# Performance work log

Measured on AMD Instinct MI355X. Metric: run time of the kernel, lower is better.

The kernel has to match this reference:

```python
import jax, jax.numpy as jnp
import numpy as np

B, T, E, H, HS, L, V = 128, 256, 384, 6, 64, 6, 78
FF = 4 * E  # 1536


def layer_norm(x, g, b, eps=1e-5):
    mu = jnp.mean(x, axis=-1, keepdims=True)
    var = jnp.mean((x - mu) ** 2, axis=-1, keepdims=True)
    return (x - mu) * jax.lax.rsqrt(var + eps) * g + b


def setup_inputs() -> dict:
    key = jax.random.key(0)
    ks = jax.random.split(key, 20)
    s = 0.02
    return {
        "context": jax.random.randint(ks[0], (B, T), 0, V),
        "tok_emb": jax.random.normal(ks[1], (V, E)) * s,
        "pos_emb": jax.random.normal(ks[2], (T, E)) * s,
        "ln1_g": jnp.ones((L, E)), "ln1_b": jnp.zeros((L, E)),
        "w_qkv": jax.random.normal(ks[3], (L, H, E, 3 * HS)) * s,  # per-head qkv, no bias
        "w_proj": jax.random.normal(ks[4], (L, E, E)) * s,
        "b_proj": jnp.zeros((L, E)),
        "ln2_g": jnp.ones((L, E)), "ln2_b": jnp.zeros((L, E)),
        "w1": jax.random.normal(ks[5], (L, E, FF)) * s, "b1": jnp.zeros((L, FF)),
        "w2": jax.random.normal(ks[6], (L, FF, E)) * s, "b2": jnp.zeros((L, E)),
        "lnf_g": jnp.ones((E,)), "lnf_b": jnp.zeros((E,)),
        "w_head": jax.random.normal(ks[7], (E, V)) * s, "b_head": jnp.zeros((V,)),
    }


def reference(context, tok_emb, pos_emb, ln1_g, ln1_b, w_qkv, w_proj, b_proj,
              ln2_g, ln2_b, w1, b1, w2, b2, lnf_g, lnf_b, w_head, b_head):
    x = tok_emb[context] + pos_emb[None, :, :]            # [B,T,E]
    causal = jnp.tril(jnp.ones((T, T), dtype=bool))       # lower-tri mask
    scale = HS ** (-0.5)
    for l in range(L):
        # multi-head attention (pre-LN), per-head qkv projection, no bias
        xn = layer_norm(x, ln1_g[l], ln1_b[l])
        qkv = jnp.einsum('bte,hef->bthf', xn, w_qkv[l])   # [B,T,H,3*HS]
        q, k, v = jnp.split(qkv, 3, axis=-1)              # each [B,T,H,HS]
        scores = jnp.einsum('bthd,bshd->bhts', q, k) * scale
        scores = jnp.where(causal, scores, -jnp.inf)
        att = jax.nn.softmax(scores, axis=-1)             # [B,H,T,T]
        o = jnp.einsum('bhts,bshd->bthd', att, v).reshape(B, T, E)
        x = x + o @ w_proj[l] + b_proj[l]
        # feed-forward (pre-LN)
        xn2 = layer_norm(x, ln2_g[l], ln2_b[l])
        x = x + jax.nn.relu(xn2 @ w1[l] + b1[l]) @ w2[l] + b2[l]
    x = layer_norm(x, lnf_g, lnf_b)
    return x @ w_head + b_head                            # [B,T,V]
```

## Files before the change

kernel.cpp:

```cpp
#include <hip/hip_runtime.h>


#define Bc 128
#define Tc 256
#define Ec 384
#define Hc 6
#define HSc 64
#define Lc 6
#define Vc 78
#define FFc 1536
#define Mc (Bc * Tc)

typedef unsigned short u16;
using bf16x8 = __attribute__((ext_vector_type(8))) short;
using f32x4 = __attribute__((ext_vector_type(4))) float;

__device__ __forceinline__ float b2f(u16 u) {
    union { float f; unsigned int i; } x;
    x.i = ((unsigned int)u) << 16;
    return x.f;
}
__device__ __forceinline__ u16 f2b(float f) {
    union { float f; unsigned int u; } x;
    x.f = f;
    unsigned int r = x.u + 0x7fffu + ((x.u >> 16) & 1u);
    return (u16)(r >> 16);
}

__device__ __forceinline__ void gload_lds16(const u16* g, u16* l) {
    __builtin_amdgcn_global_load_lds(
        (const __attribute__((address_space(1))) unsigned int*)g,
        (__attribute__((address_space(3))) unsigned int*)l, 16, 0, 0);
}

__global__ __launch_bounds__(256) void poison_kernel(
    float* __restrict__ out, int n, float val) {
    int i = blockIdx.x * 256 + threadIdx.x;
    if (i < n) out[i] = val;
}

__global__ __launch_bounds__(256) void trans_qkv_kernel(
    const float* __restrict__ in, u16* __restrict__ out) {
    int i = blockIdx.x * 256 + threadIdx.x;
    if (i >= Lc * Hc * Ec * 192) return;
    int f = i % 192;
    int r = i / 192;
    int e = r % Ec; r /= Ec;
    int h = r % Hc;
    int l = r / Hc;
    out[((size_t)l * 1152 + h * 192 + f) * Ec + e] = f2b(in[i]);
}
__global__ __launch_bounds__(256) void trans_w_kernel(
    const float* __restrict__ in, u16* __restrict__ out, int K, int N) {
    int i = blockIdx.x * 256 + threadIdx.x;
    if (i >= Lc * K * N) return;
    int n = i % N;
    int r = i / N;
    int k = r % K;
    int l = r / K;
    out[((size_t)l * N + n) * K + k] = f2b(in[i]);
}
__global__ __launch_bounds__(256) void trans_head_kernel(
    const float* __restrict__ in, u16* __restrict__ out) {
    int i = blockIdx.x * 256 + threadIdx.x;
    if (i >= Ec * Vc) return;
    int v = i % Vc, e = i / Vc;
    out[(size_t)v * Ec + e] = f2b(in[i]);
}

__global__ __launch_bounds__(256) void embed_kernel(
    const int* __restrict__ ctx, const float* __restrict__ tok,
    const float* __restrict__ pos, float* __restrict__ x) {
    int i = blockIdx.x * 256 + threadIdx.x;
    if (i >= Mc * 96) return;
    int c4 = (i % 96) * 4, bt = i / 96, t = bt % Tc;
    f32x4 tv = *reinterpret_cast<const f32x4*>(&tok[ctx[bt] * Ec + c4]);
    f32x4 pv = *reinterpret_cast<const f32x4*>(&pos[t * Ec + c4]);
    *reinterpret_cast<f32x4*>(&x[(size_t)bt * Ec + c4]) = tv + pv;
}

__global__ __launch_bounds__(256) void ln_kernel(
    const float* __restrict__ X, u16* __restrict__ Y,
    const float* __restrict__ g, const float* __restrict__ b, int nrows) {
    int row = blockIdx.x * 4 + (threadIdx.x >> 6);
    int lane = threadIdx.x & 63;
    if (row >= nrows) return;
    const float* xr = X + (size_t)row * Ec;
    float2 v[3];
    float s = 0.f;
#pragma unroll
    for (int i = 0; i < 3; ++i) {
        v[i] = *reinterpret_cast<const float2*>(&xr[2 * lane + 128 * i]);
        s += v[i].x + v[i].y;
    }
#pragma unroll
    for (int off = 32; off >= 1; off >>= 1) s += __shfl_xor(s, off, 64);
    float mean = s * (1.0f / Ec);
    float s2 = 0.f;
#pragma unroll
    for (int i = 0; i < 3; ++i) {
        float dx = v[i].x - mean, dy = v[i].y - mean;
        s2 += dx * dx + dy * dy;
    }
#pragma unroll
    for (int off = 32; off >= 1; off >>= 1) s2 += __shfl_xor(s2, off, 64);
    float rstd = rsqrtf(s2 * (1.0f / Ec) + 1e-5f);
    u16* yr = Y + (size_t)row * Ec;
#pragma unroll
    for (int i = 0; i < 3; ++i) {
        int e = 2 * lane + 128 * i;
        float2 gv = *reinterpret_cast<const float2*>(&g[e]);
        float2 bv = *reinterpret_cast<const float2*>(&b[e]);
        ushort2 ov;
        ov.x = f2b((v[i].x - mean) * rstd * gv.x + bv.x);
        ov.y = f2b((v[i].y - mean) * rstd * gv.y + bv.y);
        *reinterpret_cast<ushort2*>(&yr[e]) = ov;
    }
}

template <bool RELU, bool RESID, bool OUTBF16, bool VECEPI, bool PIPE3>
__global__ __launch_bounds__(256) void mfma_gemm(
    const u16* __restrict__ A, const u16* __restrict__ Wt,
    const float* __restrict__ bias, const float* R, void* C,
    int K, int ldC, int NV) {
    constexpr bool SWAP = VECEPI;
    __shared__ __align__(16) u16 smem[PIPE3 ? 24576 : 16384];
    int tid = threadIdx.x;

    int nwg = gridDim.x * gridDim.y;
    int bid = blockIdx.y * gridDim.x + blockIdx.x;
    int q = nwg >> 3, r = nwg & 7;
    int xcd = bid & 7, idx = bid >> 3;
    int swz = (xcd < r ? xcd * (q + 1) : r * (q + 1) + (xcd - r) * q) + idx;
    int bx = swz % gridDim.x, by = swz / gridDim.x;
    int m0 = by * 128, n0 = bx * 128;

    int w = tid >> 6, lane = tid & 63;
    int wm = (w >> 1) * 64, wn = (w & 1) * 64;
    int r16 = lane & 15, quad = lane >> 4;

    f32x4 acc[4][4] = {};

    if constexpr (PIPE3) {
        u16(*As3)[128][32] = (u16(*)[128][32])smem;
        u16(*Bs3)[128][32] = (u16(*)[128][32])(smem + 3 * 128 * 32);
        int rA = 2 * w * 16 + (lane >> 2);
        int colsw = ((lane & 3) ^ ((lane >> 3) & 3)) * 8;
        const u16* a0 = A + (size_t)(m0 + rA) * K + colsw;
        const u16* a1 = A + (size_t)(m0 + rA + 16) * K + colsw;
        const u16* b0 = Wt + (size_t)(n0 + rA) * K + colsw;
        const u16* b1 = Wt + (size_t)(n0 + rA + 16) * K + colsw;

        auto stage3 = [&](int buf, int t) {
            int k0 = t * 32;
            gload_lds16(a0 + k0, &As3[buf][2 * w * 16][0]);
            gload_lds16(a1 + k0, &As3[buf][2 * w * 16 + 16][0]);
            gload_lds16(b0 + k0, &Bs3[buf][2 * w * 16][0]);
            gload_lds16(b1 + k0, &Bs3[buf][2 * w * 16 + 16][0]);
        };
        int csw = (quad ^ ((r16 >> 1) & 3)) * 8;
        auto compute3 = [&](int buf) {
            bf16x8 af[4], bf[4];
#pragma unroll
            for (int i = 0; i < 4; ++i) {
                af[i] = *reinterpret_cast<const bf16x8*>(
                    &As3[buf][wm + i * 16 + r16][csw]);
                bf[i] = *reinterpret_cast<const bf16x8*>(
                    &Bs3[buf][wn + i * 16 + r16][csw]);
            }
#pragma unroll
            for (int mi = 0; mi < 4; ++mi)
#pragma unroll
                for (int ni = 0; ni < 4; ++ni) {
                    if (SWAP)
                        acc[mi][ni] = __builtin_amdgcn_mfma_f32_16x16x32_bf16(
                            bf[ni], af[mi], acc[mi][ni], 0, 0, 0);
                    else
                        acc[mi][ni] = __builtin_amdgcn_mfma_f32_16x16x32_bf16(
                            af[mi], bf[ni], acc[mi][ni], 0, 0, 0);
                }
        };

        int nt = K >> 5;
        stage3(0, 0);
        stage3(1, 1);
        int buf = 0;
        for (int t = 0; t < nt - 1; ++t) {
            asm volatile("s_waitcnt vmcnt(4)" ::: "memory");
            __builtin_amdgcn_s_barrier();
            __builtin_amdgcn_sched_barrier(0);
            if (t + 2 < nt) {
                int b2 = buf + 2;
                if (b2 >= 3) b2 -= 3;
                stage3(b2, t + 2);
            }
            compute3(buf);
            buf = (buf == 2) ? 0 : buf + 1;
        }
        asm volatile("s_waitcnt vmcnt(0)" ::: "memory");
        __builtin_amdgcn_s_barrier();
        __builtin_amdgcn_sched_barrier(0);
        compute3(buf);
    } else {
        u16(*As)[64] = (u16(*)[64])smem;
        u16(*Bs)[64] = (u16(*)[64])(smem + 128 * 64);
        int lrow = lane >> 3;
        int scol = ((lane & 7) ^ lrow) * 8;
        const u16* ap[4];
        const u16* bp[4];
#pragma unroll
        for (int j = 0; j < 4; ++j) {
            int row = (w * 4 + j) * 8 + lrow;
            ap[j] = A + (size_t)(m0 + row) * K + scol;
            bp[j] = Wt + (size_t)(n0 + row) * K + scol;
        }
        for (int k0 = 0; k0 < K; k0 += 64) {
            __syncthreads();
#pragma unroll
            for (int j = 0; j < 4; ++j) {
                gload_lds16(ap[j], &As[(w * 4 + j) * 8][0]);
                gload_lds16(bp[j], &Bs[(w * 4 + j) * 8][0]);
                ap[j] += 64;
                bp[j] += 64;
            }
            __syncthreads();
#pragma unroll
            for (int kk = 0; kk < 2; ++kk) {
                int csw = ((kk * 4 + quad) ^ (r16 & 7)) * 8;
                bf16x8 af[4], bf[4];
#pragma unroll
                for (int i = 0; i < 4; ++i) {
                    af[i] = *reinterpret_cast<const bf16x8*>(
                        &As[wm + i * 16 + r16][csw]);
                    bf[i] = *reinterpret_cast<const bf16x8*>(
                        &Bs[wn + i * 16 + r16][csw]);
                }
#pragma unroll
                for (int mi = 0; mi < 4; ++mi)
#pragma unroll
                    for (int ni = 0; ni < 4; ++ni) {
                        if (SWAP)
                            acc[mi][ni] = __builtin_amdgcn_mfma_f32_16x16x32_bf16(
                                bf[ni], af[mi], acc[mi][ni], 0, 0, 0);
                        else
                            acc[mi][ni] = __builtin_amdgcn_mfma_f32_16x16x32_bf16(
                                af[mi], bf[ni], acc[mi][ni], 0, 0, 0);
                    }
            }
        }
    }

    if (VECEPI && OUTBF16) {
        f32x4 bv4[4];
#pragma unroll
        for (int ni = 0; ni < 4; ++ni) {
            int gn = n0 + wn + ni * 16 + quad * 4;
            if (bias)
                bv4[ni] = *reinterpret_cast<const f32x4*>(&bias[gn]);
            else
                bv4[ni] = f32x4{0.f, 0.f, 0.f, 0.f};
        }
        __syncthreads();
#pragma unroll
        for (int mi = 0; mi < 4; ++mi) {
            int row = wm + mi * 16 + r16;
#pragma unroll
            for (int ni = 0; ni < 4; ++ni) {
                int colb = wn + ni * 16 + quad * 4;
                f32x4 v = acc[mi][ni] + bv4[ni];
                if (RELU) {
#pragma unroll
                    for (int e = 0; e < 4; ++e) v[e] = fmaxf(v[e], 0.f);
                }
                ushort4 ov;
                ov.x = f2b(v[0]);
                ov.y = f2b(v[1]);
                ov.z = f2b(v[2]);
                ov.w = f2b(v[3]);
                int pc = (colb >> 3) ^ (row & 15);
                *reinterpret_cast<ushort4*>(
                    &smem[row * 128 + pc * 8 + (colb & 7)]) = ov;
            }
        }
        __syncthreads();
        u16* cp = (u16*)C;
#pragma unroll
        for (int i = 0; i < 4; ++i) {
            int row = (tid >> 3) + 32 * i;
#pragma unroll
            for (int h = 0; h < 2; ++h) {
                int lc = (tid & 7) + 8 * h;
                int pc = lc ^ (row & 15);
                bf16x8 val = *reinterpret_cast<const bf16x8*>(
                    &smem[row * 128 + pc * 8]);
                *reinterpret_cast<bf16x8*>(
                    &cp[(size_t)(m0 + row) * ldC + n0 + lc * 8]) = val;
            }
        }
    } else if (VECEPI) {
        float* cp = (float*)C;
        f32x4 bv4[4];
#pragma unroll
        for (int ni = 0; ni < 4; ++ni) {
            int gn = n0 + wn + ni * 16 + quad * 4;
            if (bias)
                bv4[ni] = *reinterpret_cast<const f32x4*>(&bias[gn]);
            else
                bv4[ni] = f32x4{0.f, 0.f, 0.f, 0.f};
        }
#pragma unroll
        for (int mi = 0; mi < 4; ++mi) {
            int gm = m0 + wm + mi * 16 + r16;
#pragma unroll
            for (int ni = 0; ni < 4; ++ni) {
                int gn = n0 + wn + ni * 16 + quad * 4;
                size_t goff = (size_t)gm * ldC + gn;
                f32x4 v = acc[mi][ni] + bv4[ni];
                if (RELU) {
#pragma unroll
                    for (int e = 0; e < 4; ++e) v[e] = fmaxf(v[e], 0.f);
                }
                if (RESID) v += *reinterpret_cast<const f32x4*>(&R[goff]);
                *reinterpret_cast<f32x4*>(&cp[goff]) = v;
            }
        }
    } else {
#pragma unroll
        for (int mi = 0; mi < 4; ++mi)
#pragma unroll
            for (int ni = 0; ni < 4; ++ni) {
                int gn = n0 + wn + ni * 16 + r16;
                if (gn >= NV) continue;
                float bvs = bias ? bias[gn] : 0.f;
#pragma unroll
                for (int reg = 0; reg < 4; ++reg) {
                    int gm = m0 + wm + mi * 16 + quad * 4 + reg;
                    float v = acc[mi][ni][reg] + bvs;
                    if (RESID) v += R[(size_t)gm * ldC + gn];
                    if (RELU) v = fmaxf(v, 0.f);
                    if (OUTBF16)
                        ((u16*)C)[(size_t)gm * ldC + gn] = f2b(v);
                    else
                        ((float*)C)[(size_t)gm * ldC + gn] = v;
                }
            }
    }
}

__global__ __launch_bounds__(256) void attn_kernel(
    const u16* __restrict__ qkv, u16* __restrict__ o) {
    __shared__ u16 Qs[64][72];
    __shared__ u16 Ks[64][72];
    __shared__ u16 Vt[64][72];
    __shared__ u16 Ps[4][16][72];
    int tid = threadIdx.x;
    int tt = blockIdx.x, h = blockIdx.y, b = blockIdx.z;
    int w = tid >> 6, lane = tid & 63;
    int r16 = lane & 15, quad = lane >> 4;
    int t0 = tt * 64;
    const u16* base = qkv + (size_t)b * Tc * 1152 + h * 192;

    int sr = tid >> 2, sd = (tid & 3) * 16;
    {
        const u16* src = base + (size_t)(t0 + sr) * 1152 + sd;
        *reinterpret_cast<uint4*>(&Qs[sr][sd]) =
            *reinterpret_cast<const uint4*>(src);
        *reinterpret_cast<uint4*>(&Qs[sr][sd + 8]) =
            *reinterpret_cast<const uint4*>(src + 8);
    }
    __syncthreads();
    bf16x8 aq0 = *reinterpret_cast<const bf16x8*>(&Qs[w * 16 + r16][quad * 8]);
    bf16x8 aq1 = *reinterpret_cast<const bf16x8*>(&Qs[w * 16 + r16][32 + quad * 8]);

    uint4 kr0, kr1, vr0, vr1;
    {
        const u16* ks = base + (size_t)sr * 1152 + 64 + sd;
        kr0 = *reinterpret_cast<const uint4*>(ks);
        kr1 = *reinterpret_cast<const uint4*>(ks + 8);
        const u16* vs = base + (size_t)sr * 1152 + 128 + sd;
        vr0 = *reinterpret_cast<const uint4*>(vs);
        vr1 = *reinterpret_cast<const uint4*>(vs + 8);
    }
    int vslot = sr & 7, vchk = sr >> 3;

    float m_run[4], l_run[4];
#pragma unroll
    for (int r = 0; r < 4; ++r) { m_run[r] = -3.0e38f; l_run[r] = 0.f; }
    f32x4 acc_o[4] = {};

    for (int st = 0; st <= tt; ++st) {
        __syncthreads();
        {
            *reinterpret_cast<uint4*>(&Ks[sr][sd]) = kr0;
            *reinterpret_cast<uint4*>(&Ks[sr][sd + 8]) = kr1;
            u16 tv[16];
            *reinterpret_cast<uint4*>(tv) = vr0;
            *reinterpret_cast<uint4*>(tv + 8) = vr1;
#pragma unroll
            for (int j = 0; j < 16; ++j) {
                int row = sd + j;
                int pc = vchk ^ ((row >> 3) & 7);
                Vt[row][pc * 8 + vslot] = tv[j];
            }
        }
        __syncthreads();
        if (st < tt) {
            const u16* ks = base + (size_t)((st + 1) * 64 + sr) * 1152 + 64 + sd;
            kr0 = *reinterpret_cast<const uint4*>(ks);
            kr1 = *reinterpret_cast<const uint4*>(ks + 8);
            const u16* vs = base + (size_t)((st + 1) * 64 + sr) * 1152 + 128 + sd;
            vr0 = *reinterpret_cast<const uint4*>(vs);
            vr1 = *reinterpret_cast<const uint4*>(vs + 8);
        }

        f32x4 acc_s[4] = {};
#pragma unroll
        for (int ni = 0; ni < 4; ++ni) {
            bf16x8 bk0 = *reinterpret_cast<const bf16x8*>(&Ks[ni * 16 + r16][quad * 8]);
            bf16x8 bk1 = *reinterpret_cast<const bf16x8*>(&Ks[ni * 16 + r16][32 + quad * 8]);
            acc_s[ni] = __builtin_amdgcn_mfma_f32_16x16x32_bf16(aq0, bk0, acc_s[ni], 0, 0, 0);
            acc_s[ni] = __builtin_amdgcn_mfma_f32_16x16x32_bf16(aq1, bk1, acc_s[ni], 0, 0, 0);
        }

        float sc[4][4];
        float mt[4] = {-3.0e38f, -3.0e38f, -3.0e38f, -3.0e38f};
#pragma unroll
        for (int ni = 0; ni < 4; ++ni)
#pragma unroll
            for (int reg = 0; reg < 4; ++reg) {
                int col = st * 64 + ni * 16 + r16;
                int row = t0 + w * 16 + quad * 4 + reg;
                float v = (col <= row) ? acc_s[ni][reg] * 0.125f : -3.0e38f;
                sc[ni][reg] = v;
                mt[reg] = fmaxf(mt[reg], v);
            }
#pragma unroll
        for (int reg = 0; reg < 4; ++reg) {
#pragma unroll
            for (int off = 1; off <= 8; off <<= 1)
                mt[reg] = fmaxf(mt[reg], __shfl_xor(mt[reg], off, 64));
        }
        float alpha[4], lt[4];
#pragma unroll
        for (int reg = 0; reg < 4; ++reg) {
            float m_new = fmaxf(m_run[reg], mt[reg]);
            alpha[reg] = __expf(m_run[reg] - m_new);
            m_run[reg] = m_new;
            lt[reg] = 0.f;
        }
#pragma unroll
        for (int ni = 0; ni < 4; ++ni)
#pragma unroll
            for (int reg = 0; reg < 4; ++reg) {
                float p = __expf(sc[ni][reg] - m_run[reg]);
                lt[reg] += p;
                Ps[w][quad * 4 + reg][ni * 16 + r16] = f2b(p);
            }
#pragma unroll
        for (int reg = 0; reg < 4; ++reg) {
#pragma unroll
            for (int off = 1; off <= 8; off <<= 1)
                lt[reg] += __shfl_xor(lt[reg], off, 64);
            l_run[reg] = l_run[reg] * alpha[reg] + lt[reg];
        }
#pragma unroll
        for (int ni = 0; ni < 4; ++ni)
#pragma unroll
            for (int reg = 0; reg < 4; ++reg) acc_o[ni][reg] *= alpha[reg];
        __syncthreads();

        bf16x8 ap0 = *reinterpret_cast<const bf16x8*>(&Ps[w][r16][quad * 8]);
        bf16x8 ap1 = *reinterpret_cast<const bf16x8*>(&Ps[w][r16][32 + quad * 8]);
#pragma unroll
        for (int ni = 0; ni < 4; ++ni) {
            int vrow = ni * 16 + r16;
            int vx = (vrow >> 3) & 7;
            bf16x8 bv0 = *reinterpret_cast<const bf16x8*>(
                &Vt[vrow][(quad ^ vx) * 8]);
            bf16x8 bv1 = *reinterpret_cast<const bf16x8*>(
                &Vt[vrow][((quad + 4) ^ vx) * 8]);
            acc_o[ni] = __builtin_amdgcn_mfma_f32_16x16x32_bf16(ap0, bv0, acc_o[ni], 0, 0, 0);
            acc_o[ni] = __builtin_amdgcn_mfma_f32_16x16x32_bf16(ap1, bv1, acc_o[ni], 0, 0, 0);
        }
    }

    float inv[4];
#pragma unroll
    for (int reg = 0; reg < 4; ++reg) inv[reg] = 1.0f / l_run[reg];
#pragma unroll
    for (int ni = 0; ni < 4; ++ni)
#pragma unroll
        for (int reg = 0; reg < 4; ++reg) {
            int t = t0 + w * 16 + quad * 4 + reg;
            o[((size_t)b * Tc + t) * Ec + h * 64 + ni * 16 + r16] =
                f2b(acc_o[ni][reg] * inv[reg]);
        }
}

#define GRD(n) dim3(((n) + 255) / 256)

extern "C" void kernel_launch(void* const* d_in, const int* in_sizes, int n_in,
                              void* d_out, int out_size, void* d_ws, size_t ws_size,
                              hipStream_t stream) {
    const int* ctx = (const int*)d_in[0];
    const float* tok = (const float*)d_in[1];
    const float* pos = (const float*)d_in[2];
    const float* ln1g = (const float*)d_in[3];
    const float* ln1b = (const float*)d_in[4];
    const float* wqkv = (const float*)d_in[5];
    const float* wproj = (const float*)d_in[6];
    const float* bproj = (const float*)d_in[7];
    const float* ln2g = (const float*)d_in[8];
    const float* ln2b = (const float*)d_in[9];
    const float* w1 = (const float*)d_in[10];
    const float* b1 = (const float*)d_in[11];
    const float* w2 = (const float*)d_in[12];
    const float* b2 = (const float*)d_in[13];
    const float* lnfg = (const float*)d_in[14];
    const float* lnfb = (const float*)d_in[15];
    const float* whead = (const float*)d_in[16];
    const float* bhead = (const float*)d_in[17];
    float* out = (float*)d_out;

    char* ws = (char*)d_ws;
    float* x = (float*)ws;
    size_t off = (size_t)Mc * Ec * 4;
    u16* wqkvT = (u16*)(ws + off); off += (size_t)Lc * 1152 * 384 * 2;
    u16* wprojT = (u16*)(ws + off); off += (size_t)Lc * 384 * 384 * 2;
    u16* w1T = (u16*)(ws + off); off += (size_t)Lc * 1536 * 384 * 2;
    u16* w2T = (u16*)(ws + off); off += (size_t)Lc * 384 * 1536 * 2;
    u16* wheadT = (u16*)(ws + off); off += (size_t)128 * 384 * 2;
    const size_t per_b = (size_t)Tc * (Ec + 1152 + Ec + FFc) * 2;
    if (ws_size < off + per_b) {
        poison_kernel<<<GRD(out_size), 256, 0, stream>>>(out, out_size, 200.0f);
        return;
    }
    int CB = (int)((ws_size - off) / per_b);
    if (CB > Bc) CB = Bc;
    u16* xn_c = (u16*)(ws + off);
    u16* qkv_c = xn_c + (size_t)CB * Tc * Ec;
    u16* o_c = qkv_c + (size_t)CB * Tc * 1152;
    u16* ff_c = o_c + (size_t)CB * Tc * Ec;

    trans_qkv_kernel<<<GRD(Lc * Hc * Ec * 192), 256, 0, stream>>>(wqkv, wqkvT);
    trans_w_kernel<<<GRD(Lc * Ec * Ec), 256, 0, stream>>>(wproj, wprojT, Ec, Ec);
    trans_w_kernel<<<GRD(Lc * Ec * FFc), 256, 0, stream>>>(w1, w1T, Ec, FFc);
    trans_w_kernel<<<GRD(Lc * FFc * Ec), 256, 0, stream>>>(w2, w2T, FFc, Ec);
    hipMemsetAsync(wheadT, 0, (size_t)128 * 384 * 2, stream);
    trans_head_kernel<<<GRD(Ec * Vc), 256, 0, stream>>>(whead, wheadT);

    embed_kernel<<<GRD(Mc * 96), 256, 0, stream>>>(ctx, tok, pos, x);

    for (int l = 0; l < Lc; ++l) {
        for (int b0 = 0; b0 < Bc; b0 += CB) {
            int bcnt = (Bc - b0 < CB) ? (Bc - b0) : CB;
            int rows = bcnt * Tc;
            float* xc = x + (size_t)b0 * Tc * Ec;
            ln_kernel<<<rows / 4, 256, 0, stream>>>(
                xc, xn_c, ln1g + l * Ec, ln1b + l * Ec, rows);
            mfma_gemm<false, false, true, true, true><<<dim3(1152 / 128, rows / 128), 256, 0, stream>>>(
                xn_c, wqkvT + (size_t)l * 1152 * 384, nullptr, nullptr, qkv_c,
                384, 1152, 1152);
            attn_kernel<<<dim3(Tc / 64, Hc, bcnt), 256, 0, stream>>>(qkv_c, o_c);
            mfma_gemm<false, true, false, true, true><<<dim3(Ec / 128, rows / 128), 256, 0, stream>>>(
                o_c, wprojT + (size_t)l * 384 * 384, bproj + l * Ec, xc, xc,
                384, Ec, Ec);
            ln_kernel<<<rows / 4, 256, 0, stream>>>(
                xc, xn_c, ln2g + l * Ec, ln2b + l * Ec, rows);
            mfma_gemm<true, false, true, true, true><<<dim3(FFc / 128, rows / 128), 256, 0, stream>>>(
                xn_c, w1T + (size_t)l * 1536 * 384, b1 + l * FFc, nullptr, ff_c,
                384, FFc, FFc);
            mfma_gemm<false, true, false, true, true><<<dim3(Ec / 128, rows / 128), 256, 0, stream>>>(
                ff_c, w2T + (size_t)l * 384 * 1536, b2 + l * Ec, xc, xc,
                1536, Ec, Ec);
        }
    }
    for (int b0 = 0; b0 < Bc; b0 += CB) {
        int bcnt = (Bc - b0 < CB) ? (Bc - b0) : CB;
        int rows = bcnt * Tc;
        float* xc = x + (size_t)b0 * Tc * Ec;
        ln_kernel<<<rows / 4, 256, 0, stream>>>(xc, xn_c, lnfg, lnfb, rows);
        mfma_gemm<false, false, false, false, false><<<dim3(1, rows / 128), 256, 0, stream>>>(
            xn_c, wheadT, bhead, nullptr, out + (size_t)b0 * Tc * Vc,
            384, Vc, Vc);
    }
}
```

Before: 2.148 ms.

## Enlarge PIPE3 GEMM tile to 256x128 with 512-thread workgroups

The pipelined MFMA GEMM now uses a 256-row M tile with 8 waves (512 threads), so each workgroup reuses its B tile across twice as many rows. The three-stage LDS buffers grow to hold the larger A tile, and each wave issues three global-to-LDS loads per stage instead of four, with the waitcnt adjusted to match. The intent is to cut redundant weight-tile traffic and the number of workgroups. In exchange it uses more LDS per block, which may lower occupancy, and it halves the grid, which could underfill the GPU for the small N=384 GEMMs.

```diff
diff --git a/kernel.cpp b/kernel.cpp
--- a/kernel.cpp
+++ b/kernel.cpp
@@ -118,13 +118,15 @@
     }
 }
 
-template <bool RELU, bool RESID, bool OUTBF16, bool VECEPI, bool PIPE3>
-__global__ __launch_bounds__(256) void mfma_gemm(
+template <bool RELU, bool RESID, bool OUTBF16, bool VECEPI, bool PIPE3,
+          int TPB>
+__global__ __launch_bounds__(TPB) void mfma_gemm(
     const u16* __restrict__ A, const u16* __restrict__ Wt,
     const float* __restrict__ bias, const float* R, void* C,
     int K, int ldC, int NV) {
     constexpr bool SWAP = VECEPI;
-    __shared__ __align__(16) u16 smem[PIPE3 ? 24576 : 16384];
+    constexpr int BM = PIPE3 ? 256 : 128;
+    __shared__ __align__(16) u16 smem[PIPE3 ? 36864 : 16384];
     int tid = threadIdx.x;
 
     int nwg = gridDim.x * gridDim.y;
@@ -133,40 +135,52 @@
     int xcd = bid & 7, idx = bid >> 3;
     int swz = (xcd < r ? xcd * (q + 1) : r * (q + 1) + (xcd - r) * q) + idx;
     int bx = swz % gridDim.x, by = swz / gridDim.x;
-    int m0 = by * 128, n0 = bx * 128;
+    int m0 = by * BM, n0 = bx * 128;
 
     int w = tid >> 6, lane = tid & 63;
-    int wm = (w >> 1) * 64, wn = (w & 1) * 64;
+    int wm = PIPE3 ? (w >> 1) * 64 : (w >> 1) * 64;
+    int wn = (w & 1) * 64;
     int r16 = lane & 15, quad = lane >> 4;
 
     f32x4 acc[4][4] = {};
 
     if constexpr (PIPE3) {
-        u16(*As3)[128][32] = (u16(*)[128][32])smem;
-        u16(*Bs3)[128][32] = (u16(*)[128][32])(smem + 3 * 128 * 32);
-        int rA = 2 * w * 16 + (lane >> 2);
         int colsw = ((lane & 3) ^ ((lane >> 3) & 3)) * 8;
-        const u16* a0 = A + (size_t)(m0 + rA) * K + colsw;
-        const u16* a1 = A + (size_t)(m0 + rA + 16) * K + colsw;
-        const u16* b0 = Wt + (size_t)(n0 + rA) * K + colsw;
-        const u16* b1 = Wt + (size_t)(n0 + rA + 16) * K + colsw;
+        const u16* p[3];
+        u16* dst0[3];
+        int bstride[3];
+#pragma unroll
+        for (int j = 0; j < 3; ++j) {
+            int c = 3 * w + j;
+            if (c < 16) {
+                p[j] = A + (size_t)(m0 + 16 * c + (lane >> 2)) * K + colsw;
+                dst0[j] = smem + 16 * c * 32;
+                bstride[j] = 256 * 32;
+            } else {
+                int cb = c - 16;
+                p[j] = Wt + (size_t)(n0 + 16 * cb + (lane >> 2)) * K + colsw;
+                dst0[j] = smem + 3 * 256 * 32 + 16 * cb * 32;
+                bstride[j] = 128 * 32;
+            }
+        }
 
         auto stage3 = [&](int buf, int t) {
             int k0 = t * 32;
-            gload_lds16(a0 + k0, &As3[buf][2 * w * 16][0]);
-            gload_lds16(a1 + k0, &As3[buf][2 * w * 16 + 16][0]);
-            gload_lds16(b0 + k0, &Bs3[buf][2 * w * 16][0]);
-            gload_lds16(b1 + k0, &Bs3[buf][2 * w * 16 + 16][0]);
+#pragma unroll
+            for (int j = 0; j < 3; ++j)
+                gload_lds16(p[j] + k0, dst0[j] + buf * bstride[j]);
         };
         int csw = (quad ^ ((r16 >> 1) & 3)) * 8;
         auto compute3 = [&](int buf) {
+            const u16* Ab = smem + buf * (256 * 32);
+            const u16* Bb = smem + 3 * 256 * 32 + buf * (128 * 32);
             bf16x8 af[4], bf[4];
 #pragma unroll
             for (int i = 0; i < 4; ++i) {
                 af[i] = *reinterpret_cast<const bf16x8*>(
-                    &As3[buf][wm + i * 16 + r16][csw]);
+                    &Ab[(wm + i * 16 + r16) * 32 + csw]);
                 bf[i] = *reinterpret_cast<const bf16x8*>(
-                    &Bs3[buf][wn + i * 16 + r16][csw]);
+                    &Bb[(wn + i * 16 + r16) * 32 + csw]);
             }
 #pragma unroll
             for (int mi = 0; mi < 4; ++mi)
@@ -186,7 +200,7 @@
         stage3(1, 1);
         int buf = 0;
         for (int t = 0; t < nt - 1; ++t) {
-            asm volatile("s_waitcnt vmcnt(4)" ::: "memory");
+            asm volatile("s_waitcnt vmcnt(3)" ::: "memory");
             __builtin_amdgcn_s_barrier();
             __builtin_amdgcn_sched_barrier(0);
             if (t + 2 < nt) {
@@ -284,9 +298,11 @@
         }
         __syncthreads();
         u16* cp = (u16*)C;
-#pragma unroll
-        for (int i = 0; i < 4; ++i) {
-            int row = (tid >> 3) + 32 * i;
+        constexpr int RPI = TPB / 8;
+        constexpr int NIT = BM / RPI;
+#pragma unroll
+        for (int i = 0; i < NIT; ++i) {
+            int row = (tid >> 3) + RPI * i;
 #pragma unroll
             for (int h = 0; h < 2; ++h) {
                 int lc = (tid & 7) + 8 * h;
@@ -558,19 +574,19 @@
             float* xc = x + (size_t)b0 * Tc * Ec;
             ln_kernel<<<rows / 4, 256, 0, stream>>>(
                 xc, xn_c, ln1g + l * Ec, ln1b + l * Ec, rows);
-            mfma_gemm<false, false, true, true, true><<<dim3(1152 / 128, rows / 128), 256, 0, stream>>>(
+            mfma_gemm<false, false, true, true, true, 512><<<dim3(1152 / 128, rows / 256), 512, 0, stream>>>(
                 xn_c, wqkvT + (size_t)l * 1152 * 384, nullptr, nullptr, qkv_c,
                 384, 1152, 1152);
             attn_kernel<<<dim3(Tc / 64, Hc, bcnt), 256, 0, stream>>>(qkv_c, o_c);
-            mfma_gemm<false, true, false, true, true><<<dim3(Ec / 128, rows / 128), 256, 0, stream>>>(
+            mfma_gemm<false, true, false, true, true, 512><<<dim3(Ec / 128, rows / 256), 512, 0, stream>>>(
                 o_c, wprojT + (size_t)l * 384 * 384, bproj + l * Ec, xc, xc,
                 384, Ec, Ec);
             ln_kernel<<<rows / 4, 256, 0, stream>>>(
                 xc, xn_c, ln2g + l * Ec, ln2b + l * Ec, rows);
-            mfma_gemm<true, false, true, true, true><<<dim3(FFc / 128, rows / 128), 256, 0, stream>>>(
+            mfma_gemm<true, false, true, true, true, 512><<<dim3(FFc / 128, rows / 256), 512, 0, stream>>>(
                 xn_c, w1T + (size_t)l * 1536 * 384, b1 + l * FFc, nullptr, ff_c,
                 384, FFc, FFc);
-            mfma_gemm<false, true, false, true, true><<<dim3(Ec / 128, rows / 128), 256, 0, stream>>>(
+            mfma_gemm<false, true, false, true, true, 512><<<dim3(Ec / 128, rows / 256), 512, 0, stream>>>(
                 ff_c, w2T + (size_t)l * 384 * 1536, b2 + l * Ec, xc, xc,
                 1536, Ec, Ec);
         }
@@ -580,7 +596,7 @@
         int rows = bcnt * Tc;
         float* xc = x + (size_t)b0 * Tc * Ec;
         ln_kernel<<<rows / 4, 256, 0, stream>>>(xc, xn_c, lnfg, lnfb, rows);
-        mfma_gemm<false, false, false, false, false><<<dim3(1, rows / 128), 256, 0, stream>>>(
+        mfma_gemm<false, false, false, false, false, 256><<<dim3(1, rows / 128), 256, 0, stream>>>(
             xn_c, wheadT, bhead, nullptr, out + (size_t)b0 * Tc * Vc,
             384, Vc, Vc);
     }
```

Measured after the change: 2.378 ms. 1.11x slower.
